# Optimization experiments

Measured on AMD Instinct MI355X. Metric: run time of the kernel, lower is better.

The kernel has to match this reference:

```python
import jax, jax.numpy as jnp
import numpy as np

DN = ('NCDHW', 'OIDHW', 'NCDHW')

def conv(x, w, stride=1):
    k = w.shape[-1]
    pad = 'VALID' if k == 2 else 'SAME'  # ks=2,s=2 Minkowski offsets {0,1}; ks=3 centered; ks=1 pointwise
    return jax.lax.conv_general_dilated(x, w, (stride,) * 3, pad, dimension_numbers=DN)

def masked_bn(x, m, eps=1e-5):
    # BatchNorm over occupied voxels only (MinkowskiBatchNorm semantics); affine is identity at init.
    cnt = jnp.maximum(jnp.sum(m), 1.0)
    mean = jnp.sum(x * m, axis=(0, 2, 3, 4)) / cnt
    xc = (x - mean.reshape(1, -1, 1, 1, 1)) * m  # also zeroes unoccupied sites
    var = jnp.sum(xc * xc, axis=(0, 2, 3, 4)) / cnt
    return xc * jax.lax.rsqrt(var + eps).reshape(1, -1, 1, 1, 1)

def downmask(m):
    B, _, D, H, W = m.shape
    return m.reshape(B, 1, D // 2, 2, H // 2, 2, W // 2, 2).max(axis=(3, 5, 7))

def cbr(x, m, w):
    return jax.nn.relu(masked_bn(conv(x, w), m))

def res(x, m, wa, wb, wsk):
    y = masked_bn(conv(jax.nn.relu(masked_bn(conv(x, wa), m)), wb), m)
    sk = x if wsk is None else masked_bn(conv(x, wsk), m)
    return jax.nn.relu(y + sk)

def stage(x, m, wd, wa1, wb1, wsk, wa2, wb2):
    m2 = downmask(m)  # output coord set of ks=2,s=2 sparse conv
    x = jax.nn.relu(masked_bn(conv(x, wd, 2), m2))  # BasicConvolutionBlock
    x = res(x, m2, wa1, wb1, wsk)
    x = res(x, m2, wa2, wb2, None)
    return x, m2

def _forward(feats, mask, ws0, ws1, d1, a11, b11, a12, b12, d2, a21, b21, k2, a22, b22,
             d3, a31, b31, k3, a32, b32, d4, a41, b41, k4, a42, b42):
    m = mask
    x = cbr(feats * m, m, ws0)
    x = cbr(x, m, ws1)
    x, m = stage(x, m, d1, a11, b11, None, a12, b12)   # 32 -> 32 (identity skip)
    x, m = stage(x, m, d2, a21, b21, k2, a22, b22)     # 32 -> 64
    x, m = stage(x, m, d3, a31, b31, k3, a32, b32)     # 64 -> 128
    x, m = stage(x, m, d4, a41, b41, k4, a42, b42)     # 128 -> 256
    return x

def setup_inputs() -> dict:
    key = jax.random.key(0)
    ks = jax.random.split(key, 28)
    def W(k, o, i, s):
        return jax.random.normal(k, (o, i, s, s, s), jnp.float32) / np.sqrt(i * s ** 3)
    feats = jax.random.normal(ks[0], (2, 3, 64, 64, 64), jnp.float32)
    mask = (jax.random.uniform(ks[1], (2, 1, 64, 64, 64)) < 0.1).astype(jnp.float32)
    return dict(
        feats=feats * mask, mask=mask,
        ws0=W(ks[2], 32, 3, 3), ws1=W(ks[3], 32, 32, 3),
        d1=W(ks[4], 32, 32, 2), a11=W(ks[5], 32, 32, 3), b11=W(ks[6], 32, 32, 3),
        a12=W(ks[7], 32, 32, 3), b12=W(ks[8], 32, 32, 3),
        d2=W(ks[9], 32, 32, 2), a21=W(ks[10], 64, 32, 3), b21=W(ks[11], 64, 64, 3),
        k2=W(ks[12], 64, 32, 1), a22=W(ks[13], 64, 64, 3), b22=W(ks[14], 64, 64, 3),
        d3=W(ks[15], 64, 64, 2), a31=W(ks[16], 128, 64, 3), b31=W(ks[17], 128, 128, 3),
        k3=W(ks[18], 128, 64, 1), a32=W(ks[19], 128, 128, 3), b32=W(ks[20], 128, 128, 3),
        d4=W(ks[21], 128, 128, 2), a41=W(ks[22], 256, 128, 3), b41=W(ks[23], 256, 256, 3),
        k4=W(ks[24], 256, 128, 1), a42=W(ks[25], 256, 256, 3), b42=W(ks[26], 256, 256, 3))

def reference(feats, mask, ws0, ws1, d1, a11, b11, a12, b12, d2, a21, b21, k2, a22, b22,
              d3, a31, b31, k3, a32, b32, d4, a41, b41, k4, a42, b42):
    return _forward(feats, mask, ws0, ws1, d1, a11, b11, a12, b12, d2, a21, b21, k2, a22, b22,
                    d3, a31, b31, k3, a32, b32, d4, a41, b41, k4, a42, b42)
```

## Files before the change

### kernel.cpp

```cpp
#include <hip/hip_runtime.h>

#define BLK 256

static inline int gup(long work) { return (int)((work + BLK - 1) / BLK); }

__device__ inline bool occ_pred(const float* mask, const int* fmap,
                                int i, int DHW, int Ho, int Wo, int mode) {
  if (mode == 0) return mask[i] > 0.f;
  int b = i / DHW, sp = i - b * DHW;
  int HW = Ho * Wo;
  int z = sp / HW, r = sp - z * HW, y = r / Wo, x = r - y * Wo;
  int Hi = 2 * Ho, Wi = 2 * Wo;
  const int* mb = fmap + b * 8 * DHW;
  int base = ((2 * z) * Hi + 2 * y) * Wi + 2 * x;
  bool occ = false;
  for (int dz = 0; dz < 2; dz++)
    for (int dy = 0; dy < 2; dy++)
      for (int dx = 0; dx < 2; dx++)
        occ |= mb[base + dz * Hi * Wi + dy * Wi + dx] >= 0;
  return occ;
}

__global__ __launch_bounds__(1024) void cnt_k(const float* mask, const int* fmap,
    int* bcnt, int DHW, int Ho, int Wo, int mode, int total) {
  int i = blockIdx.x * 1024 + threadIdx.x;
  bool occ = (i < total) && occ_pred(mask, fmap, i, DHW, Ho, Wo, mode);
  unsigned long long bal = __ballot(occ);
  __shared__ int ws[16];
  int lane = threadIdx.x & 63, wid = threadIdx.x >> 6;
  if (lane == 0) ws[wid] = __popcll(bal);
  __syncthreads();
  if (threadIdx.x == 0) {
    int a = 0;
    for (int w = 0; w < 16; w++) a += ws[w];
    bcnt[blockIdx.x] = a;
  }
}

__global__ __launch_bounds__(1024) void scan_k(int* bcnt, int nb, int* cnt) {
  __shared__ int sh[1024];
  int t = threadIdx.x;
  int v = (t < nb) ? bcnt[t] : 0;
  sh[t] = v;
  __syncthreads();
  for (int o = 1; o < 1024; o <<= 1) {
    int u = (t >= o) ? sh[t - o] : 0;
    __syncthreads();
    sh[t] += u;
    __syncthreads();
  }
  if (t < nb) bcnt[t] = sh[t] - v;
  if (t == 0) *cnt = sh[1023];
}

__global__ __launch_bounds__(1024) void emit_k(const float* mask, const int* fmap,
    const int* boff, int* map, int* list, int DHW, int Ho, int Wo, int mode, int total) {
  int i = blockIdx.x * 1024 + threadIdx.x;
  bool occ = (i < total) && occ_pred(mask, fmap, i, DHW, Ho, Wo, mode);
  unsigned long long bal = __ballot(occ);
  int lane = threadIdx.x & 63, wid = threadIdx.x >> 6;
  __shared__ int wcnt[16], woff[16];
  if (lane == 0) wcnt[wid] = __popcll(bal);
  __syncthreads();
  if (threadIdx.x == 0) {
    int a = boff[blockIdx.x];
    for (int w = 0; w < 16; w++) { woff[w] = a; a += wcnt[w]; }
  }
  __syncthreads();
  if (i < total) {
    if (occ) {
      int p = woff[wid] + __popcll(bal & ((1ull << lane) - 1ull));
      map[i] = p; list[p] = i;
    } else map[i] = -1;
  }
}

__global__ __launch_bounds__(1024) void compact1_k(const int* __restrict__ fmap,
    int* __restrict__ map, int* __restrict__ list, int* __restrict__ cntp,
    int Do, int Ho, int Wo) {
  int DHW = Do * Ho * Wo, total = 2 * DHW;
  int tid = threadIdx.x, lane = tid & 63, wid = tid >> 6;
  bool occ = (tid < total) && occ_pred(nullptr, fmap, tid, DHW, Ho, Wo, 1);
  unsigned long long bal = __ballot(occ);
  __shared__ int wcnt[16], woff[16];
  if (lane == 0) wcnt[wid] = __popcll(bal);
  __syncthreads();
  if (tid == 0) {
    int a = 0;
    for (int w = 0; w < 16; w++) { woff[w] = a; a += wcnt[w]; }
    *cntp = a;
  }
  __syncthreads();
  if (tid < total) {
    if (occ) {
      int p = woff[wid] + __popcll(bal & ((1ull << lane) - 1ull));
      map[tid] = p; list[p] = tid;
    } else map[tid] = -1;
  }
}

__global__ __launch_bounds__(256) void csr_both_k(
    const int* __restrict__ list, const int* __restrict__ map,
    const int* __restrict__ cntp, const int* __restrict__ fmap,
    int* __restrict__ csr27, int* __restrict__ csr8,
    int D, int H, int W, int do8) {
  int n = *cntp;
  int DHW = D * H * W;
  for (int v = blockIdx.x * 256 + threadIdx.x; v < n; v += gridDim.x * 256) {
    int idx = list[v];
    int b = idx / DHW, sp = idx - b * DHW;
    int z = sp / (H * W), r = sp - z * H * W, y = r / W, x = r - y * W;
    const int* mb = map + b * DHW;
    int* e = csr27 + (long)v * 28;
    int cnt = 0;
    for (int k = 0; k < 27; k++) {
      int dz = k / 9 - 1, dy = (k / 3) % 3 - 1, dx = k % 3 - 1;
      int zz = z + dz, yy = y + dy, xx = x + dx;
      if ((unsigned)zz >= (unsigned)D || (unsigned)yy >= (unsigned)H ||
          (unsigned)xx >= (unsigned)W) continue;
      int j = mb[(zz * H + yy) * W + xx];
      if (j >= 0) e[++cnt] = (k << 24) | j;
    }
    e[0] = cnt;
    for (int s = cnt + 1; s <= 27; s++) e[s] = -1;
    if (do8) {
      int Hi = 2 * H, Wi = 2 * W;
      const int* fb = fmap + b * 8 * DHW;
      int* e8 = csr8 + (long)v * 9;
      int c8 = 0;
      for (int k = 0; k < 8; k++) {
        int dz = k >> 2, dy = (k >> 1) & 1, dx = k & 1;
        int j = fb[((2 * z + dz) * Hi + 2 * y + dy) * Wi + 2 * x + dx];
        if (j >= 0) e8[++c8] = (k << 24) | j;
      }
      e8[0] = c8;
      for (int s = c8 + 1; s <= 8; s++) e8[s] = -1;
    }
  }
}

struct WAll {
  const float* src[25];
  float* dst[25];
  int O[25], I[25], K[25];
  int sb[26];
};

__global__ __launch_bounds__(256) void wtr_all_k(WAll wa) {
  int b = blockIdx.x;
  int w = 0;
  while (w < 24 && b >= wa.sb[w + 1]) ++w;
  int O = wa.O[w], I = wa.I[w], K = wa.K[w];
  int I4 = (I + 3) >> 2;
  long tot = (long)K * I4 * O * 4;
  long t = (long)(b - wa.sb[w]) * 256 + threadIdx.x;
  if (t >= tot) return;
  int e = (int)(t & 3); long r = t >> 2;
  int co = (int)(r % O); long r2 = r / O;
  int ci4 = (int)(r2 % I4); int k = (int)(r2 / I4);
  int ci = 4 * ci4 + e;
  wa.dst[w][t] = (ci < I) ? wa.src[w][((long)co * I + ci) * K + k] : 0.f;
}

__global__ void gather0_k(const float* __restrict__ feats, const int* __restrict__ list,
                          const int* __restrict__ cntp, float* __restrict__ rows, int DHW) {
  int n = *cntp;
  int t = blockIdx.x * BLK + threadIdx.x;
  if (t >= n * 4) return;
  int vox = t >> 2, c = t & 3;
  int idx = list[vox]; int b = idx / DHW, sp = idx - b * DHW;
  rows[t] = (c < 3) ? feats[(b * 3 + c) * DHW + sp] : 0.f;
}

template <int CIN, int COUT, int CPT, int VX, int NT, bool PRE>
__global__ __launch_bounds__(256) void convk_k(
    const float* __restrict__ fin, const float* __restrict__ wt,
    float* __restrict__ fout, const int* __restrict__ csr,
    const int* __restrict__ cntp, const int* __restrict__ pcntp,
    const float* __restrict__ pslot, float* __restrict__ slot) {
  constexpr int CL = COUT / CPT;
  constexpr int G = 256 / CL;
  constexpr int VT = G * VX;
  constexpr int C4 = CIN / 4;
  constexpr int RST = C4 + 1;
  constexpr int WSZ = C4 * COUT;
  __shared__ int jtab[VT * NT];
  __shared__ float4 rbuf[VT * RST];
  __shared__ float4 wbuf[WSZ];
  __shared__ float aP[PRE ? CIN : 4], bP[PRE ? CIN : 4];
  __shared__ float swA[256], swB[256];
  int n = *cntp;
  int vb = blockIdx.x * VT;
  if (vb >= n) return;
  int tid = threadIdx.x;
  if constexpr (PRE) {
    int np = *pcntp;
    float c = fmaxf((float)np, 1.f);
    for (int ch = tid; ch < CIN; ch += 256) {
      float s = 0.f, q = 0.f;
      #pragma unroll
      for (int r = 0; r < 4; r++) { s += pslot[r * 512 + ch]; q += pslot[r * 512 + 256 + ch]; }
      float mean = s / c, var = fmaxf(q / c - mean * mean, 0.f);
      float a = rsqrtf(var + 1e-5f);
      aP[ch] = a; bP[ch] = -mean * a;
    }
  }
  for (int u = tid; u < VT * NT; u += 256) jtab[u] = -1;
  __syncthreads();
  for (int u = tid; u < VT * (NT + 1); u += 256) {
    int v = u / (NT + 1), s = u - v * (NT + 1);
    if (s > 0 && vb + v < n) {
      int e = csr[(long)(vb + v) * (NT + 1) + s];
      if (e >= 0) jtab[v * NT + (e >> 24)] = e & 0xFFFFFF;
    }
  }
  int cl = tid % CL, g = tid / CL, vg = g * VX;
  float acc[VX][CPT];
  #pragma unroll
  for (int vx = 0; vx < VX; vx++)
    #pragma unroll
    for (int m = 0; m < CPT; m++) acc[vx][m] = 0.f;
  const float4* fin4 = (const float4*)fin;
  const float4* w4 = (const float4*)wt;
  for (int k = 0; k < NT; k++) {
    __syncthreads();
    for (int u = tid; u < WSZ; u += 256) wbuf[u] = w4[(long)k * WSZ + u];
    for (int u = tid; u < VT * C4; u += 256) {
      int v = u / C4, c4 = u - v * C4;
      int j = jtab[v * NT + k];
      float4 val = make_float4(0.f, 0.f, 0.f, 0.f);
      if (j >= 0) {
        val = fin4[(long)j * C4 + c4];
        if constexpr (PRE) {
          int ch = 4 * c4;
          val.x = fmaxf(val.x * aP[ch] + bP[ch], 0.f);
          val.y = fmaxf(val.y * aP[ch + 1] + bP[ch + 1], 0.f);
          val.z = fmaxf(val.z * aP[ch + 2] + bP[ch + 2], 0.f);
          val.w = fmaxf(val.w * aP[ch + 3] + bP[ch + 3], 0.f);
        }
      }
      rbuf[v * RST + c4] = val;
    }
    __syncthreads();
    #pragma unroll
    for (int c4 = 0; c4 < C4; c4++) {
      float4 w_[CPT];
      #pragma unroll
      for (int m = 0; m < CPT; m++) w_[m] = wbuf[c4 * COUT + cl + m * CL];
      #pragma unroll
      for (int vx = 0; vx < VX; vx++) {
        float4 rv = rbuf[(vg + vx) * RST + c4];
        #pragma unroll
        for (int m = 0; m < CPT; m++)
          acc[vx][m] += rv.x * w_[m].x + rv.y * w_[m].y + rv.z * w_[m].z + rv.w * w_[m].w;
      }
    }
  }
  #pragma unroll
  for (int vx = 0; vx < VX; vx++) {
    int v = vb + vg + vx;
    if (v < n) {
      #pragma unroll
      for (int m = 0; m < CPT; m++)
        fout[(long)v * COUT + cl + m * CL] = acc[vx][m];
    }
  }
  int lane = tid & 63, wid = tid >> 6;
  #pragma unroll
  for (int m = 0; m < CPT; m++) {
    float ps = 0.f, pq = 0.f;
    #pragma unroll
    for (int vx = 0; vx < VX; vx++) {
      if (vb + vg + vx < n) { ps += acc[vx][m]; pq += acc[vx][m] * acc[vx][m]; }
    }
    #pragma unroll
    for (int o = 32; o >= CL; o >>= 1) {
      ps += __shfl_down(ps, o);
      pq += __shfl_down(pq, o);
    }
    if (lane < CL) {
      swA[(m * 4 + wid) * CL + lane] = ps;
      swB[(m * 4 + wid) * CL + lane] = pq;
    }
  }
  __syncthreads();
  if (tid < COUT) {
    int m = tid / CL, c2 = tid % CL;
    float s = 0.f, q = 0.f;
    #pragma unroll
    for (int w = 0; w < 4; w++) {
      s += swA[(m * 4 + w) * CL + c2];
      q += swB[(m * 4 + w) * CL + c2];
    }
    float* sl = slot + (blockIdx.x & 3) * 512;
    atomicAdd(&sl[tid], s);
    atomicAdd(&sl[256 + tid], q);
  }
}

template <int CIN, int COUT, int COT, int VT, int KSP, bool PRE>
__global__ __launch_bounds__(256) void convw_k(
    const float* __restrict__ fin, const float* __restrict__ wt,
    float* __restrict__ fout, const int* __restrict__ csr,
    const int* __restrict__ cntp, const int* __restrict__ pcntp,
    const float* __restrict__ pslot) {
  constexpr int CL = COT / 2;
  constexpr int G = 256 / CL;
  constexpr int VX = VT / G;
  constexpr int C4 = CIN / 4;
  constexpr int RST = C4 + 1;
  __shared__ float4 wbuf[C4 * COT];
  __shared__ float4 rbuf[VT * RST];
  __shared__ int jt[VT * 27];
  __shared__ int act[27];
  __shared__ float aP[PRE ? CIN : 4], bP[PRE ? CIN : 4];
  int n = *cntp;
  int vb = blockIdx.x * VT;
  if (vb >= n) return;
  int tid = threadIdx.x;
  int c0 = blockIdx.y * COT;
  if constexpr (PRE) {
    int np = *pcntp;
    float c = fmaxf((float)np, 1.f);
    for (int ch = tid; ch < CIN; ch += 256) {
      float s = 0.f, q = 0.f;
      #pragma unroll
      for (int r = 0; r < 4; r++) { s += pslot[r * 512 + ch]; q += pslot[r * 512 + 256 + ch]; }
      float mean = s / c, var = fmaxf(q / c - mean * mean, 0.f);
      float a = rsqrtf(var + 1e-5f);
      aP[ch] = a; bP[ch] = -mean * a;
    }
  }
  if (tid < 27) act[tid] = 0;
  for (int u = tid; u < VT * 27; u += 256) jt[u] = -1;
  __syncthreads();
  for (int u = tid; u < VT * 28; u += 256) {
    int v = u / 28, s = u - v * 28;
    if (s > 0 && vb + v < n) {
      int e = csr[(long)(vb + v) * 28 + s];
      if (e >= 0) {
        int k = e >> 24;
        jt[v * 27 + k] = e & 0xFFFFFF;
        atomicOr(&act[k], 1);
      }
    }
  }
  __syncthreads();
  int cl = tid % CL, g = tid / CL, vg = g * VX;
  float acc[VX][2];
  #pragma unroll
  for (int vx = 0; vx < VX; vx++) { acc[vx][0] = 0.f; acc[vx][1] = 0.f; }
  const float4* fin4 = (const float4*)fin;
  const float4* w4 = (const float4*)wt;
  for (int k = blockIdx.z; k < 27; k += KSP) {
    if (!act[k]) continue;
    __syncthreads();
    for (int u = tid; u < C4 * COT; u += 256) {
      int ci4 = u / COT, co = u - ci4 * COT;
      wbuf[u] = w4[(long)k * C4 * COUT + ci4 * COUT + c0 + co];
    }
    for (int u = tid; u < VT * C4; u += 256) {
      int v = u / C4, c4 = u - v * C4;
      int j = jt[v * 27 + k];
      float4 val = make_float4(0.f, 0.f, 0.f, 0.f);
      if (j >= 0) {
        val = fin4[(long)j * C4 + c4];
        if constexpr (PRE) {
          int ch = 4 * c4;
          val.x = fmaxf(val.x * aP[ch] + bP[ch], 0.f);
          val.y = fmaxf(val.y * aP[ch + 1] + bP[ch + 1], 0.f);
          val.z = fmaxf(val.z * aP[ch + 2] + bP[ch + 2], 0.f);
          val.w = fmaxf(val.w * aP[ch + 3] + bP[ch + 3], 0.f);
        }
      }
      rbuf[v * RST + c4] = val;
    }
    __syncthreads();
    #pragma unroll 8
    for (int c4 = 0; c4 < C4; c4++) {
      float4 w0 = wbuf[c4 * COT + cl];
      float4 w1 = wbuf[c4 * COT + cl + CL];
      #pragma unroll
      for (int vx = 0; vx < VX; vx++) {
        float4 rv = rbuf[(vg + vx) * RST + c4];
        acc[vx][0] += rv.x * w0.x + rv.y * w0.y + rv.z * w0.z + rv.w * w0.w;
        acc[vx][1] += rv.x * w1.x + rv.y * w1.y + rv.z * w1.z + rv.w * w1.w;
      }
    }
  }
  #pragma unroll
  for (int vx = 0; vx < VX; vx++) {
    int v = vb + vg + vx;
    if (v < n) {
      atomicAdd(&fout[(long)v * COUT + c0 + cl], acc[vx][0]);
      atomicAdd(&fout[(long)v * COUT + c0 + cl + CL], acc[vx][1]);
    }
  }
}

template <int CIN, int COUT, int ES, bool PRE>
__global__ __launch_bounds__(256) void convc_k(
    const float* __restrict__ fin, const float* __restrict__ wt,
    float* __restrict__ fout, const int* __restrict__ csr,
    const int* __restrict__ cntp, const int* __restrict__ pcntp,
    const float* __restrict__ pslot, float* __restrict__ slot) {
  constexpr int CL = COUT / 2, G = 256 / CL, C4 = CIN / 4;
  constexpr int EST = (ES > 0) ? ES : 1;
  constexpr int CPD = PRE ? CIN : 4;
  __shared__ float4 rbuf[G * C4];
  __shared__ int se[G * EST];
  __shared__ float aP[CPD], bP[CPD];
  __shared__ float sA[256], sB[256];
  __shared__ int scmax;
  int n = *cntp;
  int vb = blockIdx.x * G;
  if (vb >= n) return;
  int tid = threadIdx.x;
  if constexpr (PRE) {
    int np = *pcntp;
    float c = fmaxf((float)np, 1.f);
    for (int ch = tid; ch < CIN; ch += 256) {
      float s = 0.f, q = 0.f;
      #pragma unroll
      for (int r = 0; r < 4; r++) { s += pslot[r * 512 + ch]; q += pslot[r * 512 + 256 + ch]; }
      float mean = s / c, var = fmaxf(q / c - mean * mean, 0.f);
      float a = rsqrtf(var + 1e-5f);
      aP[ch] = a; bP[ch] = -mean * a;
    }
  }
  int cmax;
  if constexpr (ES > 0) {
    if (tid == 0) scmax = 0;
    __syncthreads();
    for (int u = tid; u < G * ES; u += 256) {
      int v = vb + u / ES;
      int e = (v < n) ? csr[(long)vb * ES + u] : 0;
      se[u] = e;
      if ((u % ES) == 0) atomicMax(&scmax, e);
    }
    __syncthreads();
    cmax = scmax;
  } else {
    __syncthreads();
    cmax = 1;
  }
  int cl = tid % CL, g = tid / CL;
  int v = vb + g;
  bool alive = v < n;
  float a0 = 0.f, a1 = 0.f;
  const float4* fin4 = (const float4*)fin;
  const float4* w4 = (const float4*)wt;
  for (int i = 1; i <= cmax; i++) {
    __syncthreads();
    for (int u = tid; u < G * C4; u += 256) {
      int gg = u / C4, c4 = u - gg * C4;
      int pj = -1;
      if constexpr (ES > 0) {
        if (vb + gg < n && i <= se[gg * EST]) pj = se[gg * EST + i];
      } else {
        if (vb + gg < n) pj = vb + gg;
      }
      float4 val = make_float4(0.f, 0.f, 0.f, 0.f);
      if (pj >= 0) {
        int j = pj & 0xFFFFFF;
        val = fin4[(long)j * C4 + c4];
        if constexpr (PRE) {
          int ch = 4 * c4;
          val.x = fmaxf(val.x * aP[ch] + bP[ch], 0.f);
          val.y = fmaxf(val.y * aP[ch + 1] + bP[ch + 1], 0.f);
          val.z = fmaxf(val.z * aP[ch + 2] + bP[ch + 2], 0.f);
          val.w = fmaxf(val.w * aP[ch + 3] + bP[ch + 3], 0.f);
        }
      }
      rbuf[u] = val;
    }
    __syncthreads();
    int pj;
    if constexpr (ES > 0) {
      pj = (alive && i <= se[g * EST]) ? se[g * EST + i] : -1;
    } else {
      pj = alive ? v : -1;
    }
    if (pj >= 0) {
      int k = pj >> 24;
      const float4* wk = w4 + (long)k * C4 * COUT + cl;
      #pragma unroll 8
      for (int c4 = 0; c4 < C4; c4++) {
        float4 rv = rbuf[g * C4 + c4];
        float4 w0 = wk[c4 * COUT];
        float4 w1 = wk[c4 * COUT + CL];
        a0 += rv.x * w0.x + rv.y * w0.y + rv.z * w0.z + rv.w * w0.w;
        a1 += rv.x * w1.x + rv.y * w1.y + rv.z * w1.z + rv.w * w1.w;
      }
    }
  }
  if (alive) {
    fout[(long)v * COUT + cl] = a0;
    fout[(long)v * COUT + cl + CL] = a1;
  }
  __syncthreads();
  sA[tid] = alive ? a0 : 0.f; sB[tid] = alive ? a1 : 0.f;
  __syncthreads();
  for (int o = 128; o >= CL; o >>= 1) {
    if (tid < o) { sA[tid] += sA[tid + o]; sB[tid] += sB[tid + o]; }
    __syncthreads();
  }
  float s0 = 0.f, s1 = 0.f;
  if (tid < CL) { s0 = sA[tid]; s1 = sB[tid]; }
  __syncthreads();
  sA[tid] = alive ? a0 * a0 : 0.f; sB[tid] = alive ? a1 * a1 : 0.f;
  __syncthreads();
  for (int o = 128; o >= CL; o >>= 1) {
    if (tid < o) { sA[tid] += sA[tid + o]; sB[tid] += sB[tid + o]; }
    __syncthreads();
  }
  if (tid < CL) {
    float* sl = slot + (blockIdx.x & 3) * 512;
    atomicAdd(&sl[tid], s0);
    atomicAdd(&sl[tid + CL], s1);
    atomicAdd(&sl[256 + tid], sA[tid]);
    atomicAdd(&sl[256 + tid + CL], sB[tid]);
  }
}

template <int C>
__global__ __launch_bounds__(BLK) void bnred_k(const float* __restrict__ rows,
    const int* __restrict__ cntp, float* __restrict__ slot) {
  int n = *cntp;
  long tot = (long)n * C;
  int tid = threadIdx.x;
  float s = 0.f, s2 = 0.f;
  for (long t = (long)blockIdx.x * BLK + tid; t < tot; t += (long)gridDim.x * BLK) {
    float v = rows[t]; s += v; s2 += v * v;
  }
  __shared__ float sh[BLK], sh2[BLK];
  sh[tid] = s; sh2[tid] = s2;
  __syncthreads();
  for (int o = BLK / 2; o >= C; o >>= 1) {
    if (tid < o) { sh[tid] += sh[tid + o]; sh2[tid] += sh2[tid + o]; }
    __syncthreads();
  }
  if (tid < C) { atomicAdd(&slot[tid], sh[tid]); atomicAdd(&slot[256 + tid], sh2[tid]); }
}

template <int C, int MODE>
__global__ __launch_bounds__(256) void skipapp_k(
    const float* __restrict__ x, const float* __restrict__ y,
    const float* __restrict__ s1, const float* __restrict__ s2,
    const int* __restrict__ cntp, float* __restrict__ out) {
  __shared__ float a1_[C], b1_[C], a2_[C], b2_[C];
  int n = *cntp;
  int tid = threadIdx.x;
  float cnt = fmaxf((float)n, 1.f);
  for (int c = tid; c < C; c += 256) {
    float s = 0.f, q = 0.f;
    #pragma unroll
    for (int r = 0; r < 4; r++) { s += s1[r * 512 + c]; q += s1[r * 512 + 256 + c]; }
    float mean = s / cnt, var = fmaxf(q / cnt - mean * mean, 0.f);
    float a = rsqrtf(var + 1e-5f);
    a1_[c] = a; b1_[c] = -mean * a;
    if (MODE != 2) {
      s = 0.f; q = 0.f;
      #pragma unroll
      for (int r = 0; r < 4; r++) { s += s2[r * 512 + c]; q += s2[r * 512 + 256 + c]; }
      mean = s / cnt; var = fmaxf(q / cnt - mean * mean, 0.f);
      a = rsqrtf(var + 1e-5f);
      a2_[c] = a; b2_[c] = -mean * a;
    }
  }
  __syncthreads();
  constexpr int C4 = C / 4;
  long tot = (long)n * C4;
  for (long t = (long)blockIdx.x * 256 + tid; t < tot; t += (long)gridDim.x * 256) {
    int c = 4 * (int)(t % C4);
    float4 xv = ((const float4*)x)[t];
    float4 yv = ((const float4*)y)[t];
    float4 o;
    o.x = xv.x * a1_[c] + b1_[c];
    o.y = xv.y * a1_[c + 1] + b1_[c + 1];
    o.z = xv.z * a1_[c + 2] + b1_[c + 2];
    o.w = xv.w * a1_[c + 3] + b1_[c + 3];
    if (MODE == 0) {
      o.x += yv.x * a2_[c] + b2_[c];
      o.y += yv.y * a2_[c + 1] + b2_[c + 1];
      o.z += yv.z * a2_[c + 2] + b2_[c + 2];
      o.w += yv.w * a2_[c + 3] + b2_[c + 3];
    } else if (MODE == 1) {
      o.x += fmaxf(yv.x * a2_[c] + b2_[c], 0.f);
      o.y += fmaxf(yv.y * a2_[c + 1] + b2_[c + 1], 0.f);
      o.z += fmaxf(yv.z * a2_[c + 2] + b2_[c + 2], 0.f);
      o.w += fmaxf(yv.w * a2_[c + 3] + b2_[c + 3], 0.f);
    } else {
      o.x += yv.x; o.y += yv.y; o.z += yv.z; o.w += yv.w;
    }
    o.x = fmaxf(o.x, 0.f); o.y = fmaxf(o.y, 0.f);
    o.z = fmaxf(o.z, 0.f); o.w = fmaxf(o.w, 0.f);
    ((float4*)out)[t] = o;
  }
}

__global__ void scatter_k(const float* __restrict__ rows, const int* __restrict__ list,
                          const int* __restrict__ cntp, float* __restrict__ out, int DHW) {
  int n = *cntp;
  int t = blockIdx.x * BLK + threadIdx.x;
  if (t >= n * 256) return;
  int vox = t >> 8, c = t & 255;
  int idx = list[vox]; int b = idx / DHW, sp = idx - b * DHW;
  out[(b * 256 + c) * DHW + sp] = rows[t];
}

#define CAP0 81920
#define CAP1 57344
#define CAP2 8192
#define CAP3 1024
#define CAP4 128

extern "C" void kernel_launch(void* const* d_in, const int* in_sizes, int n_in,
                              void* d_out, int out_size, void* d_ws, size_t ws_size,
                              hipStream_t stream) {
  const float* feats = (const float*)d_in[0];
  const float* mask0 = (const float*)d_in[1];

  char* p = (char*)d_ws;
  auto alloc = [&](size_t bytes) { char* r = p; p += (bytes + 255) & ~255ull; return r; };

  const int tab[25][4] = {
    {2, 32, 3, 27},  {3, 32, 32, 27}, {4, 32, 32, 8},  {5, 32, 32, 27}, {6, 32, 32, 27},
    {7, 32, 32, 27}, {8, 32, 32, 27}, {9, 32, 32, 8},  {10, 64, 32, 27},{11, 64, 64, 27},
    {12, 64, 32, 1}, {13, 64, 64, 27},{14, 64, 64, 27},{15, 64, 64, 8}, {16, 128, 64, 27},
    {17, 128, 128, 27},{18, 128, 64, 1},{19, 128, 128, 27},{20, 128, 128, 27},
    {21, 128, 128, 8},{22, 256, 128, 27},{23, 256, 256, 27},{24, 256, 128, 1},
    {25, 256, 256, 27},{26, 256, 256, 27},
  };
  WAll wa;
  float* wT[27] = {nullptr};
  int blk = 0;
  for (int i = 0; i < 25; i++) {
    int idx = tab[i][0], O = tab[i][1], I = tab[i][2], K = tab[i][3];
    int I4 = (I + 3) / 4;
    long sz = (long)K * I4 * O * 4;
    wT[idx] = (float*)alloc((size_t)sz * 4);
    wa.src[i] = (const float*)d_in[idx]; wa.dst[i] = wT[idx];
    wa.O[i] = O; wa.I[i] = I; wa.K[i] = K;
    wa.sb[i] = blk; blk += (int)((sz + 255) / 256);
  }
  wa.sb[25] = blk;

  int* map0 = (int*)alloc(524288 * 4);
  int* list0 = (int*)alloc((size_t)CAP0 * 4);
  int* map1 = (int*)alloc(65536 * 4);
  int* list1 = (int*)alloc((size_t)CAP1 * 4);
  int* map2 = (int*)alloc(8192 * 4);
  int* list2 = (int*)alloc(8192 * 4);
  int* map3 = (int*)alloc(1024 * 4);
  int* list3 = (int*)alloc(1024 * 4);
  int* map4 = (int*)alloc(128 * 4);
  int* list4 = (int*)alloc(128 * 4);
  int* bcnt = (int*)alloc(1024 * 4);
  int* cnts = (int*)alloc(32 * 4);
  int* c27_0 = (int*)alloc((size_t)CAP0 * 28 * 4);
  int* c27_1 = (int*)alloc((size_t)CAP1 * 28 * 4);
  int* c8_1  = (int*)alloc((size_t)CAP1 * 9 * 4);
  int* c27_2 = (int*)alloc((size_t)CAP2 * 28 * 4);
  int* c8_2  = (int*)alloc((size_t)CAP2 * 9 * 4);
  int* c27_3 = (int*)alloc((size_t)CAP3 * 28 * 4);
  int* c8_3  = (int*)alloc((size_t)CAP3 * 9 * 4);
  int* c27_4 = (int*)alloc((size_t)CAP4 * 28 * 4);
  int* c8_4  = (int*)alloc((size_t)CAP4 * 9 * 4);
  float* stats = (float*)alloc(25 * 2048 * 4);
  float* G0  = (float*)alloc((size_t)CAP0 * 4 * 4);
  float* F0a = (float*)alloc((size_t)CAP0 * 32 * 4);
  float* F0b = (float*)alloc((size_t)CAP0 * 32 * 4);
  float *R1[4], *R2[4];
  for (int i = 0; i < 4; i++) R1[i] = (float*)alloc((size_t)CAP1 * 32 * 4);
  for (int i = 0; i < 4; i++) R2[i] = (float*)alloc((size_t)CAP2 * 64 * 4);
  size_t z3sz = (size_t)CAP3 * 128 * 4 * 6 + (size_t)CAP4 * 256 * 4 * 6;
  float* Z3 = (float*)alloc(z3sz);
  float* R3[6], *R4[6];
  for (int i = 0; i < 6; i++) R3[i] = Z3 + (size_t)i * CAP3 * 128;
  for (int i = 0; i < 6; i++) R4[i] = Z3 + (size_t)6 * CAP3 * 128 + (size_t)i * CAP4 * 256;

  hipMemsetAsync(stats, 0, 25 * 2048 * 4, stream);
  hipMemsetAsync(Z3, 0, z3sz, stream);
  hipMemsetAsync(d_out, 0, (size_t)out_size * 4, stream);

  wtr_all_k<<<blk, 256, 0, stream>>>(wa);

  int* n0 = cnts + 0; int* n1 = cnts + 1; int* n2 = cnts + 2;
  int* n3 = cnts + 3; int* n4 = cnts + 4;

  cnt_k<<<512, 1024, 0, stream>>>(mask0, nullptr, bcnt, 262144, 64, 64, 0, 524288);
  scan_k<<<1, 1024, 0, stream>>>(bcnt, 512, n0);
  emit_k<<<512, 1024, 0, stream>>>(mask0, nullptr, bcnt, map0, list0, 262144, 64, 64, 0, 524288);
  gather0_k<<<gup((long)CAP0 * 4), BLK, 0, stream>>>(feats, list0, n0, G0, 262144);
  csr_both_k<<<512, 256, 0, stream>>>(list0, map0, n0, nullptr, c27_0, nullptr, 64, 64, 64, 0);

  cnt_k<<<64, 1024, 0, stream>>>(nullptr, map0, bcnt, 32768, 32, 32, 1, 65536);
  scan_k<<<1, 1024, 0, stream>>>(bcnt, 64, n1);
  emit_k<<<64, 1024, 0, stream>>>(nullptr, map0, bcnt, map1, list1, 32768, 32, 32, 1, 65536);
  csr_both_k<<<256, 256, 0, stream>>>(list1, map1, n1, map0, c27_1, c8_1, 32, 32, 32, 1);

  cnt_k<<<8, 1024, 0, stream>>>(nullptr, map1, bcnt, 4096, 16, 16, 1, 8192);
  scan_k<<<1, 1024, 0, stream>>>(bcnt, 8, n2);
  emit_k<<<8, 1024, 0, stream>>>(nullptr, map1, bcnt, map2, list2, 4096, 16, 16, 1, 8192);
  csr_both_k<<<32, 256, 0, stream>>>(list2, map2, n2, map1, c27_2, c8_2, 16, 16, 16, 1);

  compact1_k<<<1, 1024, 0, stream>>>(map2, map3, list3, n3, 8, 8, 8);
  csr_both_k<<<4, 256, 0, stream>>>(list3, map3, n3, map2, c27_3, c8_3, 8, 8, 8, 1);

  compact1_k<<<1, 1024, 0, stream>>>(map3, map4, list4, n4, 4, 4, 4);
  csr_both_k<<<1, 256, 0, stream>>>(list4, map4, n4, map3, c27_4, c8_4, 4, 4, 4, 1);

  auto slot = [&](int i) { return stats + (size_t)i * 2048; };
  auto bgrid = [&](long cap, int C) { long g = (cap * C / 4 + 255) / 256; return (int)(g > 2048 ? 2048 : g); };

  {
    int g = (CAP0 + 127) / 128;
    convk_k<4, 32, 4, 4, 27, false><<<g, 256, 0, stream>>>(G0, wT[2], F0a, c27_0, n0, nullptr, nullptr, slot(0));
    convk_k<32, 32, 4, 4, 27, true><<<g, 256, 0, stream>>>(F0a, wT[3], F0b, c27_0, n0, n0, slot(0), slot(1));
  }

  {
    int g = (CAP1 + 127) / 128, ag = bgrid(CAP1, 32);
    convk_k<32, 32, 4, 4, 8, true><<<g, 256, 0, stream>>>(F0b, wT[4], R1[0], c8_1, n1, n0, slot(1), slot(2));
    convk_k<32, 32, 4, 4, 27, true><<<g, 256, 0, stream>>>(R1[0], wT[5], R1[1], c27_1, n1, n1, slot(2), slot(3));
    convk_k<32, 32, 4, 4, 27, true><<<g, 256, 0, stream>>>(R1[1], wT[6], R1[2], c27_1, n1, n1, slot(3), slot(4));
    skipapp_k<32, 1><<<ag, 256, 0, stream>>>(R1[2], R1[0], slot(4), slot(2), n1, R1[3]);
    convk_k<32, 32, 4, 4, 27, false><<<g, 256, 0, stream>>>(R1[3], wT[7], R1[1], c27_1, n1, nullptr, nullptr, slot(5));
    convk_k<32, 32, 4, 4, 27, true><<<g, 256, 0, stream>>>(R1[1], wT[8], R1[2], c27_1, n1, n1, slot(5), slot(6));
    skipapp_k<32, 2><<<ag, 256, 0, stream>>>(R1[2], R1[3], slot(6), nullptr, n1, R1[0]);
  }

  {
    int g32 = (CAP2 + 31) / 32, ag = bgrid(CAP2, 64);
    convk_k<32, 32, 4, 1, 8, false><<<g32, 256, 0, stream>>>(R1[0], wT[9], R2[0], c8_2, n2, nullptr, nullptr, slot(7));
    convk_k<32, 64, 4, 2, 27, true><<<g32, 256, 0, stream>>>(R2[0], wT[10], R2[1], c27_2, n2, n2, slot(7), slot(8));
    convk_k<64, 64, 4, 2, 27, true><<<g32, 256, 0, stream>>>(R2[1], wT[11], R2[2], c27_2, n2, n2, slot(8), slot(9));
    convc_k<32, 64, 0, true><<<(CAP2 + 7) / 8, 256, 0, stream>>>(R2[0], wT[12], R2[3], nullptr, n2, n2, slot(7), slot(10));
    skipapp_k<64, 0><<<ag, 256, 0, stream>>>(R2[2], R2[3], slot(9), slot(10), n2, R2[1]);
    convk_k<64, 64, 4, 2, 27, false><<<g32, 256, 0, stream>>>(R2[1], wT[13], R2[0], c27_2, n2, nullptr, nullptr, slot(11));
    convk_k<64, 64, 4, 2, 27, true><<<g32, 256, 0, stream>>>(R2[0], wT[14], R2[2], c27_2, n2, n2, slot(11), slot(12));
    skipapp_k<64, 2><<<ag, 256, 0, stream>>>(R2[2], R2[1], slot(12), nullptr, n2, R2[3]);
  }

  {
    int gP = (CAP3 + 7) / 8, gO = (CAP3 + 3) / 4, ag = bgrid(CAP3, 128);
    int rO = gup((long)CAP3 * 128); if (rO > 512) rO = 512;
    dim3 gw(CAP3 / 16, 1, 4);
    convc_k<64, 64, 9, false><<<gP, 256, 0, stream>>>(R2[3], wT[15], R3[0], c8_3, n3, nullptr, nullptr, slot(13));
    convw_k<64, 128, 128, 16, 4, true><<<gw, 256, 0, stream>>>(R3[0], wT[16], R3[1], c27_3, n3, n3, slot(13));
    bnred_k<128><<<rO, BLK, 0, stream>>>(R3[1], n3, slot(14));
    convw_k<128, 128, 128, 16, 4, true><<<gw, 256, 0, stream>>>(R3[1], wT[17], R3[2], c27_3, n3, n3, slot(14));
    bnred_k<128><<<rO, BLK, 0, stream>>>(R3[2], n3, slot(15));
    convc_k<64, 128, 0, true><<<gO, 256, 0, stream>>>(R3[0], wT[18], R3[3], nullptr, n3, n3, slot(13), slot(16));
    skipapp_k<128, 0><<<ag, 256, 0, stream>>>(R3[2], R3[3], slot(15), slot(16), n3, R3[1]);
    convw_k<128, 128, 128, 16, 4, false><<<gw, 256, 0, stream>>>(R3[1], wT[19], R3[4], c27_3, n3, nullptr, nullptr);
    bnred_k<128><<<rO, BLK, 0, stream>>>(R3[4], n3, slot(17));
    convw_k<128, 128, 128, 16, 4, true><<<gw, 256, 0, stream>>>(R3[4], wT[20], R3[5], c27_3, n3, n3, slot(17));
    bnred_k<128><<<rO, BLK, 0, stream>>>(R3[5], n3, slot(18));
    skipapp_k<128, 2><<<ag, 256, 0, stream>>>(R3[5], R3[1], slot(18), nullptr, n3, R3[0]);
  }

  {
    int gP = (CAP4 + 3) / 4, gO = (CAP4 + 1) / 2, ag = bgrid(CAP4, 256);
    int rO = gup((long)CAP4 * 256); if (rO > 512) rO = 512;
    dim3 gw(CAP4 / 16, 4, 8);
    convc_k<128, 128, 9, false><<<gP, 256, 0, stream>>>(R3[0], wT[21], R4[0], c8_4, n4, nullptr, nullptr, slot(19));
    convw_k<128, 256, 64, 16, 8, true><<<gw, 256, 0, stream>>>(R4[0], wT[22], R4[1], c27_4, n4, n4, slot(19));
    bnred_k<256><<<rO, BLK, 0, stream>>>(R4[1], n4, slot(20));
    convw_k<256, 256, 64, 16, 8, true><<<gw, 256, 0, stream>>>(R4[1], wT[23], R4[2], c27_4, n4, n4, slot(20));
    bnred_k<256><<<rO, BLK, 0, stream>>>(R4[2], n4, slot(21));
    convc_k<128, 256, 0, true><<<gO, 256, 0, stream>>>(R4[0], wT[24], R4[3], nullptr, n4, n4, slot(19), slot(22));
    skipapp_k<256, 0><<<ag, 256, 0, stream>>>(R4[2], R4[3], slot(21), slot(22), n4, R4[1]);
    convw_k<256, 256, 64, 16, 8, false><<<gw, 256, 0, stream>>>(R4[1], wT[25], R4[4], c27_4, n4, nullptr, nullptr);
    bnred_k<256><<<rO, BLK, 0, stream>>>(R4[4], n4, slot(23));
    convw_k<256, 256, 64, 16, 8, true><<<gw, 256, 0, stream>>>(R4[4], wT[26], R4[5], c27_4, n4, n4, slot(23));
    bnred_k<256><<<rO, BLK, 0, stream>>>(R4[5], n4, slot(24));
    skipapp_k<256, 2><<<ag, 256, 0, stream>>>(R4[5], R4[1], slot(24), nullptr, n4, R4[0]);
  }

  scatter_k<<<gup((long)CAP4 * 256), BLK, 0, stream>>>(R4[0], list4, n4, (float*)d_out, 64);
}
```

Before: 1.596 ms.

## Fuse coarse-level compaction, scatter into skip kernel, merge memsets, raise MAC priority

The three coarse-level voxel compactions (levels 2-4) are merged into one single-block chain kernel, replacing cnt/scan/emit and two compact1 launches. The final scatter to the dense output is folded into the last skip-apply kernel, and the stats and Z3 memsets become one memset over a contiguous allocation. The inner MAC loops of the conv kernels are also wrapped in s_setprio. These changes mainly cut launch count and small-kernel overhead. The level-2 compaction now runs serially on a single workgroup, and the scattered output writes are uncoalesced.

```diff
diff --git a/kernel.cpp b/kernel.cpp
--- a/kernel.cpp
+++ b/kernel.cpp
@@ -75,28 +75,46 @@
   }
 }
 
-__global__ __launch_bounds__(1024) void compact1_k(const int* __restrict__ fmap,
-    int* __restrict__ map, int* __restrict__ list, int* __restrict__ cntp,
-    int Do, int Ho, int Wo) {
+__device__ void compact_lvl(const int* fmap, int* map, int* list, int* cntp,
+                            int Do, int Ho, int Wo,
+                            int* shbase, int* wcnt, int* woff) {
   int DHW = Do * Ho * Wo, total = 2 * DHW;
   int tid = threadIdx.x, lane = tid & 63, wid = tid >> 6;
-  bool occ = (tid < total) && occ_pred(nullptr, fmap, tid, DHW, Ho, Wo, 1);
-  unsigned long long bal = __ballot(occ);
-  __shared__ int wcnt[16], woff[16];
-  if (lane == 0) wcnt[wid] = __popcll(bal);
-  __syncthreads();
-  if (tid == 0) {
-    int a = 0;
-    for (int w = 0; w < 16; w++) { woff[w] = a; a += wcnt[w]; }
-    *cntp = a;
-  }
-  __syncthreads();
-  if (tid < total) {
-    if (occ) {
-      int p = woff[wid] + __popcll(bal & ((1ull << lane) - 1ull));
-      map[tid] = p; list[p] = tid;
-    } else map[tid] = -1;
-  }
+  if (tid == 0) *shbase = 0;
+  __syncthreads();
+  for (int c0 = 0; c0 < total; c0 += 1024) {
+    int i = c0 + tid;
+    bool occ = (i < total) && occ_pred(nullptr, fmap, i, DHW, Ho, Wo, 1);
+    unsigned long long bal = __ballot(occ);
+    if (lane == 0) wcnt[wid] = __popcll(bal);
+    __syncthreads();
+    if (tid == 0) {
+      int a = *shbase;
+      for (int w = 0; w < 16; w++) { woff[w] = a; a += wcnt[w]; }
+      *shbase = a;
+    }
+    __syncthreads();
+    if (i < total) {
+      if (occ) {
+        int p = woff[wid] + __popcll(bal & ((1ull << lane) - 1ull));
+        map[i] = p; list[p] = i;
+      } else map[i] = -1;
+    }
+    __syncthreads();
+  }
+  if (tid == 0) *cntp = *shbase;
+}
+
+__global__ __launch_bounds__(1024) void chain_k(const int* map1,
+    int* map2, int* list2, int* cnt2,
+    int* map3, int* list3, int* cnt3,
+    int* map4, int* list4, int* cnt4) {
+  __shared__ int sb, wcnt[16], woff[16];
+  compact_lvl(map1, map2, list2, cnt2, 16, 16, 16, &sb, wcnt, woff);
+  __syncthreads();
+  compact_lvl(map2, map3, list3, cnt3, 8, 8, 8, &sb, wcnt, woff);
+  __syncthreads();
+  compact_lvl(map3, map4, list4, cnt4, 4, 4, 4, &sb, wcnt, woff);
 }
 
 __global__ __launch_bounds__(256) void csr_both_k(
@@ -242,6 +260,7 @@
       rbuf[v * RST + c4] = val;
     }
     __syncthreads();
+    __builtin_amdgcn_s_setprio(1);
     #pragma unroll
     for (int c4 = 0; c4 < C4; c4++) {
       float4 w_[CPT];
@@ -255,6 +274,7 @@
           acc[vx][m] += rv.x * w_[m].x + rv.y * w_[m].y + rv.z * w_[m].z + rv.w * w_[m].w;
       }
     }
+    __builtin_amdgcn_s_setprio(0);
   }
   #pragma unroll
   for (int vx = 0; vx < VX; vx++) {
@@ -376,6 +396,7 @@
       rbuf[v * RST + c4] = val;
     }
     __syncthreads();
+    __builtin_amdgcn_s_setprio(1);
     #pragma unroll 8
     for (int c4 = 0; c4 < C4; c4++) {
       float4 w0 = wbuf[c4 * COT + cl];
@@ -387,6 +408,7 @@
         acc[vx][1] += rv.x * w1.x + rv.y * w1.y + rv.z * w1.z + rv.w * w1.w;
       }
     }
+    __builtin_amdgcn_s_setprio(0);
   }
   #pragma unroll
   for (int vx = 0; vx < VX; vx++) {
@@ -543,11 +565,12 @@
   if (tid < C) { atomicAdd(&slot[tid], sh[tid]); atomicAdd(&slot[256 + tid], sh2[tid]); }
 }
 
-template <int C, int MODE>
+template <int C, int MODE, int SCAT>
 __global__ __launch_bounds__(256) void skipapp_k(
     const float* __restrict__ x, const float* __restrict__ y,
     const float* __restrict__ s1, const float* __restrict__ s2,
-    const int* __restrict__ cntp, float* __restrict__ out) {
+    const int* __restrict__ cntp, float* __restrict__ out,
+    const int* __restrict__ slist) {
   __shared__ float a1_[C], b1_[C], a2_[C], b2_[C];
   int n = *cntp;
   int tid = threadIdx.x;
@@ -595,18 +618,16 @@
     }
     o.x = fmaxf(o.x, 0.f); o.y = fmaxf(o.y, 0.f);
     o.z = fmaxf(o.z, 0.f); o.w = fmaxf(o.w, 0.f);
-    ((float4*)out)[t] = o;
-  }
-}
-
-__global__ void scatter_k(const float* __restrict__ rows, const int* __restrict__ list,
-                          const int* __restrict__ cntp, float* __restrict__ out, int DHW) {
-  int n = *cntp;
-  int t = blockIdx.x * BLK + threadIdx.x;
-  if (t >= n * 256) return;
-  int vox = t >> 8, c = t & 255;
-  int idx = list[vox]; int b = idx / DHW, sp = idx - b * DHW;
-  out[(b * 256 + c) * DHW + sp] = rows[t];
+    if constexpr (SCAT) {
+      int vox = (int)(t / C4);
+      int idx = slist[vox];
+      int b = idx >> 6, sp = idx & 63;
+      float* op = out + ((long)(b * 256 + c) * 64 + sp);
+      op[0] = o.x; op[64] = o.y; op[128] = o.z; op[192] = o.w;
+    } else {
+      ((float4*)out)[t] = o;
+    }
+  }
 }
 
 #define CAP0 81920
@@ -668,20 +689,20 @@
   int* c27_4 = (int*)alloc((size_t)CAP4 * 28 * 4);
   int* c8_4  = (int*)alloc((size_t)CAP4 * 9 * 4);
   float* stats = (float*)alloc(25 * 2048 * 4);
+  size_t z3sz = (size_t)CAP3 * 128 * 4 * 6 + (size_t)CAP4 * 256 * 4 * 6;
+  float* Z3 = (float*)alloc(z3sz);
+  size_t zero_len = (size_t)((char*)Z3 - (char*)stats) + z3sz;
   float* G0  = (float*)alloc((size_t)CAP0 * 4 * 4);
   float* F0a = (float*)alloc((size_t)CAP0 * 32 * 4);
   float* F0b = (float*)alloc((size_t)CAP0 * 32 * 4);
   float *R1[4], *R2[4];
   for (int i = 0; i < 4; i++) R1[i] = (float*)alloc((size_t)CAP1 * 32 * 4);
   for (int i = 0; i < 4; i++) R2[i] = (float*)alloc((size_t)CAP2 * 64 * 4);
-  size_t z3sz = (size_t)CAP3 * 128 * 4 * 6 + (size_t)CAP4 * 256 * 4 * 6;
-  float* Z3 = (float*)alloc(z3sz);
   float* R3[6], *R4[6];
   for (int i = 0; i < 6; i++) R3[i] = Z3 + (size_t)i * CAP3 * 128;
   for (int i = 0; i < 6; i++) R4[i] = Z3 + (size_t)6 * CAP3 * 128 + (size_t)i * CAP4 * 256;
 
-  hipMemsetAsync(stats, 0, 25 * 2048 * 4, stream);
-  hipMemsetAsync(Z3, 0, z3sz, stream);
+  hipMemsetAsync(stats, 0, zero_len, stream);
   hipMemsetAsync(d_out, 0, (size_t)out_size * 4, stream);
 
   wtr_all_k<<<blk, 256, 0, stream>>>(wa);
@@ -700,15 +721,9 @@
   emit_k<<<64, 1024, 0, stream>>>(nullptr, map0, bcnt, map1, list1, 32768, 32, 32, 1, 65536);
   csr_both_k<<<256, 256, 0, stream>>>(list1, map1, n1, map0, c27_1, c8_1, 32, 32, 32, 1);
 
-  cnt_k<<<8, 1024, 0, stream>>>(nullptr, map1, bcnt, 4096, 16, 16, 1, 8192);
-  scan_k<<<1, 1024, 0, stream>>>(bcnt, 8, n2);
-  emit_k<<<8, 1024, 0, stream>>>(nullptr, map1, bcnt, map2, list2, 4096, 16, 16, 1, 8192);
+  chain_k<<<1, 1024, 0, stream>>>(map1, map2, list2, n2, map3, list3, n3, map4, list4, n4);
   csr_both_k<<<32, 256, 0, stream>>>(list2, map2, n2, map1, c27_2, c8_2, 16, 16, 16, 1);
-
-  compact1_k<<<1, 1024, 0, stream>>>(map2, map3, list3, n3, 8, 8, 8);
   csr_both_k<<<4, 256, 0, stream>>>(list3, map3, n3, map2, c27_3, c8_3, 8, 8, 8, 1);
-
-  compact1_k<<<1, 1024, 0, stream>>>(map3, map4, list4, n4, 4, 4, 4);
   csr_both_k<<<1, 256, 0, stream>>>(list4, map4, n4, map3, c27_4, c8_4, 4, 4, 4, 1);
 
   auto slot = [&](int i) { return stats + (size_t)i * 2048; };
@@ -725,10 +740,10 @@
     convk_k<32, 32, 4, 4, 8, true><<<g, 256, 0, stream>>>(F0b, wT[4], R1[0], c8_1, n1, n0, slot(1), slot(2));
     convk_k<32, 32, 4, 4, 27, true><<<g, 256, 0, stream>>>(R1[0], wT[5], R1[1], c27_1, n1, n1, slot(2), slot(3));
     convk_k<32, 32, 4, 4, 27, true><<<g, 256, 0, stream>>>(R1[1], wT[6], R1[2], c27_1, n1, n1, slot(3), slot(4));
-    skipapp_k<32, 1><<<ag, 256, 0, stream>>>(R1[2], R1[0], slot(4), slot(2), n1, R1[3]);
+    skipapp_k<32, 1, 0><<<ag, 256, 0, stream>>>(R1[2], R1[0], slot(4), slot(2), n1, R1[3], nullptr);
     convk_k<32, 32, 4, 4, 27, false><<<g, 256, 0, stream>>>(R1[3], wT[7], R1[1], c27_1, n1, nullptr, nullptr, slot(5));
     convk_k<32, 32, 4, 4, 27, true><<<g, 256, 0, stream>>>(R1[1], wT[8], R1[2], c27_1, n1, n1, slot(5), slot(6));
-    skipapp_k<32, 2><<<ag, 256, 0, stream>>>(R1[2], R1[3], slot(6), nullptr, n1, R1[0]);
+    skipapp_k<32, 2, 0><<<ag, 256, 0, stream>>>(R1[2], R1[3], slot(6), nullptr, n1, R1[0], nullptr);
   }
 
   {
@@ -737,10 +752,10 @@
     convk_k<32, 64, 4, 2, 27, true><<<g32, 256, 0, stream>>>(R2[0], wT[10], R2[1], c27_2, n2, n2, slot(7), slot(8));
     convk_k<64, 64, 4, 2, 27, true><<<g32, 256, 0, stream>>>(R2[1], wT[11], R2[2], c27_2, n2, n2, slot(8), slot(9));
     convc_k<32, 64, 0, true><<<(CAP2 + 7) / 8, 256, 0, stream>>>(R2[0], wT[12], R2[3], nullptr, n2, n2, slot(7), slot(10));
-    skipapp_k<64, 0><<<ag, 256, 0, stream>>>(R2[2], R2[3], slot(9), slot(10), n2, R2[1]);
+    skipapp_k<64, 0, 0><<<ag, 256, 0, stream>>>(R2[2], R2[3], slot(9), slot(10), n2, R2[1], nullptr);
     convk_k<64, 64, 4, 2, 27, false><<<g32, 256, 0, stream>>>(R2[1], wT[13], R2[0], c27_2, n2, nullptr, nullptr, slot(11));
     convk_k<64, 64, 4, 2, 27, true><<<g32, 256, 0, stream>>>(R2[0], wT[14], R2[2], c27_2, n2, n2, slot(11), slot(12));
-    skipapp_k<64, 2><<<ag, 256, 0, stream>>>(R2[2], R2[1], slot(12), nullptr, n2, R2[3]);
+    skipapp_k<64, 2, 0><<<ag, 256, 0, stream>>>(R2[2], R2[1], slot(12), nullptr, n2, R2[3], nullptr);
   }
 
   {
@@ -753,12 +768,12 @@
     convw_k<128, 128, 128, 16, 4, true><<<gw, 256, 0, stream>>>(R3[1], wT[17], R3[2], c27_3, n3, n3, slot(14));
     bnred_k<128><<<rO, BLK, 0, stream>>>(R3[2], n3, slot(15));
     convc_k<64, 128, 0, true><<<gO, 256, 0, stream>>>(R3[0], wT[18], R3[3], nullptr, n3, n3, slot(13), slot(16));
-    skipapp_k<128, 0><<<ag, 256, 0, stream>>>(R3[2], R3[3], slot(15), slot(16), n3, R3[1]);
+    skipapp_k<128, 0, 0><<<ag, 256, 0, stream>>>(R3[2], R3[3], slot(15), slot(16), n3, R3[1], nullptr);
     convw_k<128, 128, 128, 16, 4, false><<<gw, 256, 0, stream>>>(R3[1], wT[19], R3[4], c27_3, n3, nullptr, nullptr);
     bnred_k<128><<<rO, BLK, 0, stream>>>(R3[4], n3, slot(17));
     convw_k<128, 128, 128, 16, 4, true><<<gw, 256, 0, stream>>>(R3[4], wT[20], R3[5], c27_3, n3, n3, slot(17));
     bnred_k<128><<<rO, BLK, 0, stream>>>(R3[5], n3, slot(18));
-    skipapp_k<128, 2><<<ag, 256, 0, stream>>>(R3[5], R3[1], slot(18), nullptr, n3, R3[0]);
+    skipapp_k<128, 2, 0><<<ag, 256, 0, stream>>>(R3[5], R3[1], slot(18), nullptr, n3, R3[0], nullptr);
   }
 
   {
@@ -771,13 +786,12 @@
     convw_k<256, 256, 64, 16, 8, true><<<gw, 256, 0, stream>>>(R4[1], wT[23], R4[2], c27_4, n4, n4, slot(20));
     bnred_k<256><<<rO, BLK, 0, stream>>>(R4[2], n4, slot(21));
     convc_k<128, 256, 0, true><<<gO, 256, 0, stream>>>(R4[0], wT[24], R4[3], nullptr, n4, n4, slot(19), slot(22));
-    skipapp_k<256, 0><<<ag, 256, 0, stream>>>(R4[2], R4[3], slot(21), slot(22), n4, R4[1]);
+    skipapp_k<256, 0, 0><<<ag, 256, 0, stream>>>(R4[2], R4[3], slot(21), slot(22), n4, R4[1], nullptr);
     convw_k<256, 256, 64, 16, 8, false><<<gw, 256, 0, stream>>>(R4[1], wT[25], R4[4], c27_4, n4, nullptr, nullptr);
     bnred_k<256><<<rO, BLK, 0, stream>>>(R4[4], n4, slot(23));
     convw_k<256, 256, 64, 16, 8, true><<<gw, 256, 0, stream>>>(R4[4], wT[26], R4[5], c27_4, n4, n4, slot(23));
     bnred_k<256><<<rO, BLK, 0, stream>>>(R4[5], n4, slot(24));
-    skipapp_k<256, 2><<<ag, 256, 0, stream>>>(R4[5], R4[1], slot(24), nullptr, n4, R4[0]);
-  }
-
-  scatter_k<<<gup((long)CAP4 * 256), BLK, 0, stream>>>(R4[0], list4, n4, (float*)d_out, 64);
-}
+    skipapp_k<256, 2, 1><<<ag, 256, 0, stream>>>(R4[5], R4[1], slot(24), nullptr, n4,
+                                                 (float*)d_out, list4);
+  }
+}
```

After: 1.581 ms. About the same (-1.0%).
